# Optimization experiments

Measured on AMD Instinct MI355X. Metric: run time of the kernel, lower is better.

Reference implementation:

```python
import jax, jax.numpy as jnp
import numpy as np

N_NODES, N_EDGES, N_GRAPHS = 100000, 400000, 4096
F_NODE, F_EDGE, G = 78, 11, 256
NUM_LAYERS, NUM_TIMESTEPS = 3, 2
L = NUM_LAYERS - 1  # number of GNNLayers after GetContext


def _lrelu(x):
    return jax.nn.leaky_relu(x, 0.01)


def _seg_softmax(logits, seg, n):
    # softmax of logits grouped by segment id (edge_softmax over dst / softmax_nodes over graph)
    m = jax.ops.segment_max(logits, seg, num_segments=n)
    e = jnp.exp(logits - m[seg])
    s = jax.ops.segment_sum(e, seg, num_segments=n)
    return e / s[seg]


def _gru(x, h, Wih, Whh, bih, bhh):
    gi = x @ Wih.T + bih
    gh = h @ Whh.T + bhh
    ir, iz, inn = jnp.split(gi, 3, axis=-1)
    hr, hz, hn = jnp.split(gh, 3, axis=-1)
    r = jax.nn.sigmoid(ir + hr)
    z = jax.nn.sigmoid(iz + hz)
    nn_ = jnp.tanh(inn + r * hn)
    return (1.0 - z) * nn_ + z * h


def _forward(node_feats, edge_feats, W_pn, b_pn, W_pe1, b_pe1, W_pe2, b_pe2, W_et, b_et,
             gru0_Wih, gru0_Whh, gru0_bih, gru0_bhh,
             gnn_W_pe, gnn_b_pe, gnn_W_pn, gnn_b_pn, gnn_Wih, gnn_Whh, gnn_bih, gnn_bhh,
             ro_W_cl, ro_b_cl, ro_W_pn, ro_b_pn, ro_Wih, ro_Whh, ro_bih, ro_bhh,
             ln_gamma, ln_beta, src, dst, node_graph):
    N, B = node_feats.shape[0], N_GRAPHS
    # ---- GetContext ----
    hv_new = _lrelu(node_feats @ W_pn.T + b_pn)                                  # [N,G]
    he1 = _lrelu(jnp.concatenate([node_feats[src], edge_feats], -1) @ W_pe1.T + b_pe1)  # [E,G]
    logits = _lrelu(jnp.concatenate([hv_new[dst], he1], -1) @ W_pe2.T + b_pe2)   # [E,1]
    a = _seg_softmax(logits, dst, N)
    c = jax.ops.segment_sum(a * (he1 @ W_et.T + b_et), dst, num_segments=N)      # [N,G]
    h = jax.nn.relu(_gru(jax.nn.elu(c), hv_new, gru0_Wih, gru0_Whh, gru0_bih, gru0_bhh))
    # ---- GNNLayers (AttentiveGRU2) ----
    for l in range(L):
        lg = _lrelu(jnp.concatenate([h[dst], h[src]], -1) @ gnn_W_pe[l].T + gnn_b_pe[l])  # [E,1]
        a = _seg_softmax(lg, dst, N)
        hv = h @ gnn_W_pn[l].T + gnn_b_pn[l]
        c = jax.ops.segment_sum(a * hv[src], dst, num_segments=N)
        h = jax.nn.relu(_gru(jax.nn.elu(c), h, gnn_Wih[l], gnn_Whh[l], gnn_bih[l], gnn_bhh[l]))
    # ---- AttentiveFPReadout ----
    g_feats = jax.ops.segment_sum(h, node_graph, num_segments=B)                 # [B,G]
    for t in range(NUM_TIMESTEPS):
        z = _lrelu(jnp.concatenate([jax.nn.relu(g_feats)[node_graph], h], -1) @ ro_W_cl[t].T + ro_b_cl[t])  # [N,1]
        a = _seg_softmax(z, node_graph, B)
        hv = h @ ro_W_pn[t].T + ro_b_pn[t]
        gr = jax.ops.segment_sum(a * hv, node_graph, num_segments=B)
        g_feats = jax.nn.relu(_gru(jax.nn.elu(gr), g_feats, ro_Wih[t], ro_Whh[t], ro_bih[t], ro_bhh[t]))
    # ---- LayerNorm (dropout is identity at inference) ----
    mu = jnp.mean(g_feats, -1, keepdims=True)
    var = jnp.mean((g_feats - mu) ** 2, -1, keepdims=True)
    return (g_feats - mu) / jnp.sqrt(var + 1e-5) * ln_gamma + ln_beta


def setup_inputs() -> dict:
    key = jax.random.key(0)
    ks = iter(jax.random.split(key, 64))

    def nrm(shape, scale=1.0):
        return jax.random.normal(next(ks), shape, dtype=jnp.float32) * scale

    def lin(out_d, in_d):
        return nrm((out_d, in_d), 1.0 / np.sqrt(in_d))

    d = {}
    d['node_feats'] = nrm((N_NODES, F_NODE))
    d['edge_feats'] = nrm((N_EDGES, F_EDGE))
    d['src'] = jax.random.randint(next(ks), (N_EDGES,), 0, N_NODES)
    d['dst'] = jax.random.randint(next(ks), (N_EDGES,), 0, N_NODES)
    d['node_graph'] = jnp.sort(jax.random.randint(next(ks), (N_NODES,), 0, N_GRAPHS))
    # GetContext params
    d['W_pn'] = lin(G, F_NODE); d['b_pn'] = jnp.zeros((G,), jnp.float32)
    d['W_pe1'] = lin(G, F_NODE + F_EDGE); d['b_pe1'] = jnp.zeros((G,), jnp.float32)
    d['W_pe2'] = lin(1, 2 * G); d['b_pe2'] = jnp.zeros((1,), jnp.float32)
    d['W_et'] = lin(G, G); d['b_et'] = jnp.zeros((G,), jnp.float32)
    d['gru0_Wih'] = lin(3 * G, G); d['gru0_Whh'] = lin(3 * G, G)
    d['gru0_bih'] = jnp.zeros((3 * G,), jnp.float32); d['gru0_bhh'] = jnp.zeros((3 * G,), jnp.float32)
    # stacked GNNLayer params
    s2g = 1.0 / np.sqrt(2 * G); sg = 1.0 / np.sqrt(G)
    d['gnn_W_pe'] = nrm((L, 1, 2 * G), s2g); d['gnn_b_pe'] = jnp.zeros((L, 1), jnp.float32)
    d['gnn_W_pn'] = nrm((L, G, G), sg); d['gnn_b_pn'] = jnp.zeros((L, G), jnp.float32)
    d['gnn_Wih'] = nrm((L, 3 * G, G), sg); d['gnn_Whh'] = nrm((L, 3 * G, G), sg)
    d['gnn_bih'] = jnp.zeros((L, 3 * G), jnp.float32); d['gnn_bhh'] = jnp.zeros((L, 3 * G), jnp.float32)
    # stacked readout (GlobalPool) params
    T = NUM_TIMESTEPS
    d['ro_W_cl'] = nrm((T, 1, 2 * G), s2g); d['ro_b_cl'] = jnp.zeros((T, 1), jnp.float32)
    d['ro_W_pn'] = nrm((T, G, G), sg); d['ro_b_pn'] = jnp.zeros((T, G), jnp.float32)
    d['ro_Wih'] = nrm((T, 3 * G, G), sg); d['ro_Whh'] = nrm((T, 3 * G, G), sg)
    d['ro_bih'] = jnp.zeros((T, 3 * G), jnp.float32); d['ro_bhh'] = jnp.zeros((T, 3 * G), jnp.float32)
    d['ln_gamma'] = jnp.ones((G,), jnp.float32); d['ln_beta'] = jnp.zeros((G,), jnp.float32)
    return d


def reference(node_feats, edge_feats, src, dst, node_graph, W_pn, b_pn, W_pe1, b_pe1, W_pe2, b_pe2,
              W_et, b_et, gru0_Wih, gru0_Whh, gru0_bih, gru0_bhh,
              gnn_W_pe, gnn_b_pe, gnn_W_pn, gnn_b_pn, gnn_Wih, gnn_Whh, gnn_bih, gnn_bhh,
              ro_W_cl, ro_b_cl, ro_W_pn, ro_b_pn, ro_Wih, ro_Whh, ro_bih, ro_bhh, ln_gamma, ln_beta):
    return _forward(node_feats, edge_feats, W_pn, b_pn, W_pe1, b_pe1, W_pe2, b_pe2, W_et, b_et,
                    gru0_Wih, gru0_Whh, gru0_bih, gru0_bhh,
                    gnn_W_pe, gnn_b_pe, gnn_W_pn, gnn_b_pn, gnn_Wih, gnn_Whh, gnn_bih, gnn_bhh,
                    ro_W_cl, ro_b_cl, ro_W_pn, ro_b_pn, ro_Wih, ro_Whh, ro_bih, ro_bhh,
                    ln_gamma, ln_beta, src, dst, node_graph)
```

## Files before the change

### kernel.cpp

```cpp
#include <hip/hip_runtime.h>

#define NN 100000
#define NE 400000
#define NB 4096
#define FN 78
#define FE 11
#define GD 256
#define NL 2
#define NT 2

typedef unsigned short u16;
typedef __attribute__((ext_vector_type(8))) short bf16x8;
typedef __attribute__((ext_vector_type(4))) float f32x4;

__device__ __forceinline__ float lrelu_(float x){ return x > 0.f ? x : 0.01f*x; }
__device__ __forceinline__ float elu_(float x){ return x > 0.f ? x : expf(x) - 1.f; }
__device__ __forceinline__ float sigm_(float x){ return 1.f/(1.f + expf(-x)); }

__device__ __forceinline__ float bf2f(u16 u){ return __uint_as_float(((unsigned)u) << 16); }
__device__ __forceinline__ u16 f2bf(float f){
  unsigned u = __float_as_uint(f);
  unsigned r = (u + 0x7fffu + ((u >> 16) & 1u)) >> 16;
  return (u16)r;
}

__global__ void k_zero(float* p, size_t n){
  size_t i = (size_t)blockIdx.x*blockDim.x + threadIdx.x;
  size_t st = (size_t)gridDim.x*blockDim.x;
  for (; i < n; i += st) p[i] = 0.f;
}

__global__ void k_count(const int* __restrict__ dst, int* __restrict__ cnt, int E){
  int e = blockIdx.x*256 + threadIdx.x;
  if (e < E) atomicAdd(&cnt[dst[e]], 1);
}
__global__ void k_scan1(const int* __restrict__ cnt, int* __restrict__ part,
                        int* __restrict__ btot, int n){
  __shared__ int sd[256];
  int i = blockIdx.x*256 + threadIdx.x;
  int v = (i < n) ? cnt[i] : 0;
  sd[threadIdx.x] = v; __syncthreads();
  for (int d=1; d<256; d<<=1){
    int t = (threadIdx.x >= d) ? sd[threadIdx.x-d] : 0;
    __syncthreads();
    sd[threadIdx.x] += t;
    __syncthreads();
  }
  if (i < n) part[i] = sd[threadIdx.x];
  if (threadIdx.x == 255) btot[blockIdx.x] = sd[255];
}
__global__ void k_scan2(const int* __restrict__ btot, int* __restrict__ boff, int nb){
  __shared__ int sd[512];
  int tid = threadIdx.x;
  int v = (tid < nb) ? btot[tid] : 0;
  sd[tid] = v; __syncthreads();
  for (int d=1; d<512; d<<=1){
    int t = (tid >= d) ? sd[tid-d] : 0;
    __syncthreads();
    sd[tid] += t;
    __syncthreads();
  }
  if (tid < nb) boff[tid] = sd[tid] - v;
}
__global__ void k_scan3(const int* __restrict__ part, const int* __restrict__ boff,
                        int* __restrict__ rowptr, int n){
  int i = blockIdx.x*256 + threadIdx.x;
  if (i < n) rowptr[i+1] = part[i] + boff[blockIdx.x];
  if (i == 0) rowptr[0] = 0;
}
__global__ void k_cursor(const int* __restrict__ rowptr, int* __restrict__ cursor, int n){
  int i = blockIdx.x*256 + threadIdx.x;
  if (i < n) cursor[i] = rowptr[i];
}
__global__ void k_fill(const int* __restrict__ dst, int* __restrict__ cursor,
                       int* __restrict__ order, int E){
  int e = blockIdx.x*256 + threadIdx.x;
  if (e < E){
    int pos = atomicAdd(&cursor[dst[e]], 1);
    order[pos] = e;
  }
}
__global__ void k_gpb(const int* __restrict__ ng, int* __restrict__ gpb, int N, int B){
  int b = blockIdx.x*256 + threadIdx.x;
  if (b > B) return;
  int lo = 0, hi = N;
  while (lo < hi){ int mid = (lo+hi)>>1; if (ng[mid] < b) lo = mid+1; else hi = mid; }
  gpb[b] = lo;
}

__global__ void k_pack_b(const float* __restrict__ W, u16* __restrict__ Bp, int OUT, int K){
  int t = blockIdx.x*256 + threadIdx.x;
  if (t >= OUT*K) return;
  int j = t & 7;
  int l = (t >> 3) & 63;
  int rest = t >> 9;
  int nks = K >> 5;
  int ks = rest % nks, c = rest / nks;
  int col = c*16 + (l & 15);
  int k = ks*32 + (l >> 4)*8 + j;
  Bp[t] = f2bf(W[(size_t)col*K + k]);
}

__global__ void k_pack_b96(const float* __restrict__ W, int ldw, u16* __restrict__ Bp){
  int t = blockIdx.x*256 + threadIdx.x;
  if (t >= 256*96) return;
  int j = t & 7;
  int l = (t >> 3) & 63;
  int rest = t >> 9;
  int ks = rest % 3, c = rest / 3;
  int col = c*16 + (l & 15);
  int k = ks*32 + (l >> 4)*8 + j;
  Bp[t] = (k < FN) ? f2bf(W[(size_t)col*ldw + k]) : (u16)0;
}

__global__ void k_pack_rz(const float* __restrict__ Wih, const float* __restrict__ Whh,
                          u16* __restrict__ Bp){
  int t = blockIdx.x*256 + threadIdx.x;
  int j = t & 7;
  int l = (t >> 3) & 63;
  int rest = t >> 9;
  int ks = rest & 15, c = rest >> 4;
  int srcrow = (c & 1)*256 + (c >> 1)*16 + (l & 15);
  int k = ks*32 + (l >> 4)*8 + j;
  float v = (k < 256) ? Wih[(size_t)srcrow*GD + k] : Whh[(size_t)srcrow*GD + (k - 256)];
  Bp[t] = f2bf(v);
}

__global__ void __launch_bounds__(512)
k_np2_mfma(const float* __restrict__ nf,
           const u16* __restrict__ BpA, const float* __restrict__ bA,
           const u16* __restrict__ BpB, const float* __restrict__ bB,
           u16* __restrict__ hv, u16* __restrict__ Pb, int N){
  int tid = threadIdx.x;
  int wv = __builtin_amdgcn_readfirstlane(tid >> 6);
  int lane = tid & 63;
  int m = lane & 15, kg = lane >> 4;
  int r0 = blockIdx.x*64;
  f32x4 accA[2][4], accB[2][4];
  #pragma unroll
  for (int t=0;t<2;t++)
    #pragma unroll
    for (int rt=0;rt<4;rt++){ accA[t][rt] = (f32x4)(0.f); accB[t][rt] = (f32x4)(0.f); }
  #pragma unroll
  for (int ks=0; ks<3; ks++){
    int koff = ks*32 + kg*8;
    bf16x8 a[4];
    #pragma unroll
    for (int rt=0; rt<4; rt++){
      int row = r0 + rt*16 + m;
      if (row > N-1) row = N-1;
      const float* base = nf + (size_t)row*FN;
      #pragma unroll
      for (int q=0;q<8;q++){
        int k = koff + q;
        a[rt][q] = (short)((k < FN) ? f2bf(base[k]) : (u16)0);
      }
    }
    #pragma unroll
    for (int t=0;t<2;t++){
      int c = wv*2 + t;
      bf16x8 bva = *(const bf16x8*)&BpA[(size_t)((c*3 + ks)*64 + lane)*8];
      bf16x8 bvb = *(const bf16x8*)&BpB[(size_t)((c*3 + ks)*64 + lane)*8];
      #pragma unroll
      for (int rt=0; rt<4; rt++){
        accA[t][rt] = __builtin_amdgcn_mfma_f32_16x16x32_bf16(a[rt], bva, accA[t][rt], 0, 0, 0);
        accB[t][rt] = __builtin_amdgcn_mfma_f32_16x16x32_bf16(a[rt], bvb, accB[t][rt], 0, 0, 0);
      }
    }
  }
  #pragma unroll
  for (int t=0;t<2;t++){
    int col = wv*32 + t*16 + m;
    float ba = bA[col], bb = bB[col];
    #pragma unroll
    for (int rt=0; rt<4; rt++){
      #pragma unroll
      for (int i=0;i<4;i++){
        int row = r0 + rt*16 + kg*4 + i;
        if (row < N){
          hv[(size_t)row*GD + col] = f2bf(lrelu_(accA[t][rt][i] + ba));
          Pb[(size_t)row*GD + col] = f2bf(accB[t][rt][i] + bb);
        }
      }
    }
  }
}

__global__ void k_dot2_bf16(const u16* __restrict__ rows, const float* __restrict__ wv,
                            float* __restrict__ za, float* __restrict__ zb, int N){
  int wav = threadIdx.x >> 6, lane = threadIdx.x & 63;
  int i = blockIdx.x*4 + wav;
  if (i >= N) return;
  int c0 = lane*4;
  ushort4 r4 = *(const ushort4*)&rows[(size_t)i*GD + c0];
  float4 wa = *(const float4*)&wv[c0];
  float4 wb = *(const float4*)&wv[GD + c0];
  float v0 = bf2f(r4.x), v1 = bf2f(r4.y), v2 = bf2f(r4.z), v3 = bf2f(r4.w);
  float va = v0*wa.x + v1*wa.y + v2*wa.z + v3*wa.w;
  float vb = v0*wb.x + v1*wb.y + v2*wb.z + v3*wb.w;
  #pragma unroll
  for (int off=32; off; off>>=1){ va += __shfl_down(va, off); vb += __shfl_down(vb, off); }
  if (lane == 0){ za[i] = va; zb[i] = vb; }
}

__global__ void k_dot1_bf16(const u16* __restrict__ rows, const float* __restrict__ wv,
                            float* __restrict__ z, int N){
  int wav = threadIdx.x >> 6, lane = threadIdx.x & 63;
  int i = blockIdx.x*4 + wav;
  if (i >= N) return;
  int c0 = lane*4;
  ushort4 r4 = *(const ushort4*)&rows[(size_t)i*GD + c0];
  float4 wa = *(const float4*)&wv[c0];
  float va = bf2f(r4.x)*wa.x + bf2f(r4.y)*wa.y + bf2f(r4.z)*wa.z + bf2f(r4.w)*wa.w;
  #pragma unroll
  for (int off=32; off; off>>=1) va += __shfl_down(va, off);
  if (lane == 0) z[i] = va;
}

__global__ void k_dotg_relu(const float* __restrict__ g, const float* __restrict__ wv,
                            float* __restrict__ zg, int B){
  int wav = threadIdx.x >> 6, lane = threadIdx.x & 63;
  int i = blockIdx.x*4 + wav;
  if (i >= B) return;
  int c0 = lane*4;
  float4 gv = *(const float4*)&g[(size_t)i*GD + c0];
  float4 wa = *(const float4*)&wv[c0];
  float va = fmaxf(gv.x,0.f)*wa.x + fmaxf(gv.y,0.f)*wa.y + fmaxf(gv.z,0.f)*wa.z + fmaxf(gv.w,0.f)*wa.w;
  #pragma unroll
  for (int off=32; off; off>>=1) va += __shfl_down(va, off);
  if (lane == 0) zg[i] = va;
}

__global__ void __launch_bounds__(256)
k_ctx_fused(const u16* __restrict__ P, const float* __restrict__ za,
            const int* __restrict__ order, const int* __restrict__ rowptr,
            const int* __restrict__ src, const float* __restrict__ ef,
            const float* __restrict__ Wpe1, const float* __restrict__ bpe1,
            const float* __restrict__ Wpe2, const float* __restrict__ bpe2,
            u16* __restrict__ wc, float* __restrict__ sdeg, int N){
  int wv = threadIdx.x >> 6, lane = threadIdx.x & 63;
  int d = blockIdx.x*4 + wv;
  if (d >= N) return;
  int j0 = rowptr[d], j1 = rowptr[d+1];
  int c0 = lane*4;
  float wb0 = Wpe2[GD+c0], wb1 = Wpe2[GD+c0+1], wb2 = Wpe2[GD+c0+2], wb3 = Wpe2[GD+c0+3];
  float bp0 = bpe1[c0], bp1 = bpe1[c0+1], bp2 = bpe1[c0+2], bp3 = bpe1[c0+3];
  float wk0[FE], wk1[FE], wk2[FE], wk3[FE];
  #pragma unroll
  for (int k=0;k<FE;k++){
    wk0[k] = Wpe1[(size_t)(c0+0)*(FN+FE) + FN + k];
    wk1[k] = Wpe1[(size_t)(c0+1)*(FN+FE) + FN + k];
    wk2[k] = Wpe1[(size_t)(c0+2)*(FN+FE) + FN + k];
    wk3[k] = Wpe1[(size_t)(c0+3)*(FN+FE) + FN + k];
  }
  float zad = za[d] + bpe2[0];
  float m = -1e30f, s = 0.f;
  float a0=0.f, a1=0.f, a2=0.f, a3=0.f;
  for (int j=j0; j<j1; j++){
    int e = order[j];
    int sn = src[e];
    ushort4 p4 = *(const ushort4*)&P[(size_t)sn*GD + c0];
    const float* efp = &ef[(size_t)e*FE];
    float efv[FE];
    #pragma unroll
    for (int k=0;k<FE;k++) efv[k] = efp[k];
    float h0 = bf2f(p4.x)+bp0, h1 = bf2f(p4.y)+bp1, h2 = bf2f(p4.z)+bp2, h3 = bf2f(p4.w)+bp3;
    #pragma unroll
    for (int k=0;k<FE;k++){
      h0 += wk0[k]*efv[k]; h1 += wk1[k]*efv[k]; h2 += wk2[k]*efv[k]; h3 += wk3[k]*efv[k];
    }
    h0 = lrelu_(h0); h1 = lrelu_(h1); h2 = lrelu_(h2); h3 = lrelu_(h3);
    float part = h0*wb0 + h1*wb1 + h2*wb2 + h3*wb3;
    #pragma unroll
    for (int off=32; off; off>>=1) part += __shfl_down(part, off);
    float l = lrelu_(part + zad);
    l = __shfl(l, 0);
    float mn = fmaxf(m, l);
    float sc = __expf(m - mn);
    float p  = __expf(l - mn);
    s = s*sc + p;
    a0 = a0*sc + p*h0; a1 = a1*sc + p*h1; a2 = a2*sc + p*h2; a3 = a3*sc + p*h3;
    m = mn;
  }
  float inv = (j1 > j0) ? 1.f/s : 0.f;
  ushort4 o;
  o.x = f2bf(a0*inv); o.y = f2bf(a1*inv); o.z = f2bf(a2*inv); o.w = f2bf(a3*inv);
  *(ushort4*)&wc[(size_t)d*GD + c0] = o;
  if (lane == 0) sdeg[d] = (j1 > j0) ? 1.f : 0.f;
}

__global__ void __launch_bounds__(256)
k_gnn_fused(const u16* __restrict__ hv, const float* __restrict__ za, const float* __restrict__ zb,
            const int* __restrict__ order, const int* __restrict__ rowptr,
            const int* __restrict__ src, const float* __restrict__ bias,
            u16* __restrict__ cw, int N){
  int wv = threadIdx.x >> 6, lane = threadIdx.x & 63;
  int d = blockIdx.x*4 + wv;
  if (d >= N) return;
  int j0 = rowptr[d], j1 = rowptr[d+1];
  int c0 = lane*4;
  float zad = za[d] + bias[0];
  float M = -1e30f;
  for (int j=j0; j<j1; j++){
    int sn = src[order[j]];
    M = fmaxf(M, lrelu_(zad + zb[sn]));
  }
  float s = 0.f;
  float a0=0.f, a1=0.f, a2=0.f, a3=0.f;
  for (int j=j0; j<j1; j++){
    int e = order[j];
    int sn = src[e];
    float p = __expf(lrelu_(zad + zb[sn]) - M);
    ushort4 r4 = *(const ushort4*)&hv[(size_t)sn*GD + c0];
    s += p;
    a0 += p*bf2f(r4.x);
    a1 += p*bf2f(r4.y);
    a2 += p*bf2f(r4.z);
    a3 += p*bf2f(r4.w);
  }
  float inv = (j1 > j0) ? 1.f/s : 0.f;
  ushort4 o;
  o.x = f2bf(elu_(a0*inv)); o.y = f2bf(elu_(a1*inv));
  o.z = f2bf(elu_(a2*inv)); o.w = f2bf(elu_(a3*inv));
  *(ushort4*)&cw[(size_t)d*GD + c0] = o;
}

__global__ void __launch_bounds__(256)
k_ro_fused(const u16* __restrict__ hv, const float* __restrict__ zg, const float* __restrict__ zh,
           const int* __restrict__ gpb, const float* __restrict__ bias,
           float* __restrict__ gr, int B){
  int b = blockIdx.x, tid = threadIdx.x;
  int i0 = gpb[b], i1 = gpb[b+1];
  float zgb = zg[b] + bias[0];
  __shared__ float red[256];
  float lm = -1e30f;
  for (int i = i0 + tid; i < i1; i += 256) lm = fmaxf(lm, lrelu_(zgb + zh[i]));
  red[tid] = lm; __syncthreads();
  for (int d2=128; d2; d2>>=1){ if (tid < d2) red[tid] = fmaxf(red[tid], red[tid+d2]); __syncthreads(); }
  float M = red[0]; __syncthreads();
  float ls = 0.f;
  for (int i = i0 + tid; i < i1; i += 256) ls += __expf(lrelu_(zgb + zh[i]) - M);
  red[tid] = ls; __syncthreads();
  for (int d2=128; d2; d2>>=1){ if (tid < d2) red[tid] += red[tid+d2]; __syncthreads(); }
  float S = red[0];
  float acc = 0.f;
  for (int i = i0; i < i1; i++){
    float p = __expf(lrelu_(zgb + zh[i]) - M);
    acc += p * bf2f(hv[(size_t)i*GD + tid]);
  }
  gr[(size_t)b*GD + tid] = (i1 > i0) ? acc/S : 0.f;
}

__global__ void k_segsum_sorted(const u16* __restrict__ h, const int* __restrict__ gpb,
                                float* __restrict__ g, int B){
  int b = blockIdx.x, tid = threadIdx.x;
  int i0 = gpb[b], i1 = gpb[b+1];
  float acc = 0.f;
  for (int i = i0; i < i1; i++) acc += bf2f(h[(size_t)i*GD + tid]);
  g[(size_t)b*GD + tid] = acc;
}

__global__ void __launch_bounds__(512)
k_gru_mfma32(const u16* __restrict__ x, const u16* __restrict__ hprev,
             const u16* __restrict__ rzp, const u16* __restrict__ nip, const u16* __restrict__ nhp,
             const float* __restrict__ bih, const float* __restrict__ bhh,
             u16* __restrict__ hout, int R){
  int tid = threadIdx.x;
  int wv = __builtin_amdgcn_readfirstlane(tid >> 6);
  int lane = tid & 63;
  int m = lane & 15, kg = lane >> 4;
  int r0 = blockIdx.x*32;

  f32x4 arz[2][4], ani[2][2], anh[2][2];
  #pragma unroll
  for (int rt=0;rt<2;rt++){
    #pragma unroll
    for (int t=0;t<4;t++) arz[rt][t] = (f32x4)(0.f);
    #pragma unroll
    for (int t=0;t<2;t++){ ani[rt][t] = (f32x4)(0.f); anh[rt][t] = (f32x4)(0.f); }
  }

  #pragma unroll
  for (int ks=0; ks<8; ks++){
    int koff = ks*32 + kg*8;
    bf16x8 ax[2], ah[2];
    #pragma unroll
    for (int rt=0; rt<2; rt++){
      int row = r0 + rt*16 + m;
      ax[rt] = *(const bf16x8*)&x[(size_t)row*GD + koff];
      ah[rt] = *(const bf16x8*)&hprev[(size_t)row*GD + koff];
    }
    #pragma unroll
    for (int t=0;t<4;t++){
      int c = wv*4 + t;
      bf16x8 bx = *(const bf16x8*)&rzp[(size_t)((c*16 + ks    )*64 + lane)*8];
      bf16x8 bh = *(const bf16x8*)&rzp[(size_t)((c*16 + ks + 8)*64 + lane)*8];
      #pragma unroll
      for (int rt=0; rt<2; rt++){
        arz[rt][t] = __builtin_amdgcn_mfma_f32_16x16x32_bf16(ax[rt], bx, arz[rt][t], 0, 0, 0);
        arz[rt][t] = __builtin_amdgcn_mfma_f32_16x16x32_bf16(ah[rt], bh, arz[rt][t], 0, 0, 0);
      }
    }
    #pragma unroll
    for (int t=0;t<2;t++){
      int c = wv*2 + t;
      bf16x8 bi = *(const bf16x8*)&nip[(size_t)((c*8 + ks)*64 + lane)*8];
      bf16x8 bh = *(const bf16x8*)&nhp[(size_t)((c*8 + ks)*64 + lane)*8];
      #pragma unroll
      for (int rt=0; rt<2; rt++){
        ani[rt][t] = __builtin_amdgcn_mfma_f32_16x16x32_bf16(ax[rt], bi, ani[rt][t], 0, 0, 0);
        anh[rt][t] = __builtin_amdgcn_mfma_f32_16x16x32_bf16(ah[rt], bh, anh[rt][t], 0, 0, 0);
      }
    }
  }

  #pragma unroll
  for (int g=0; g<2; g++){
    int ch = (wv*2 + g)*16 + m;
    float brz_r = bih[ch] + bhh[ch];
    float brz_z = bih[ch+GD] + bhh[ch+GD];
    float bin   = bih[ch+2*GD];
    float bhn   = bhh[ch+2*GD];
    #pragma unroll
    for (int rt=0; rt<2; rt++){
      #pragma unroll
      for (int i=0;i<4;i++){
        int row = r0 + rt*16 + kg*4 + i;
        float rr = sigm_(arz[rt][2*g  ][i] + brz_r);
        float zz = sigm_(arz[rt][2*g+1][i] + brz_z);
        float nn = tanhf(ani[rt][g][i] + bin + rr*(anh[rt][g][i] + bhn));
        float hp = bf2f(hprev[(size_t)row*GD + ch]);
        float o = (1.f - zz)*nn + zz*hp;
        hout[(size_t)row*GD + ch] = f2bf(fmaxf(o, 0.f));
      }
    }
  }
}

template<int DO_ELU>
__global__ void __launch_bounds__(512)
k_proj_mfma64(const u16* __restrict__ X, const u16* __restrict__ Wp,
              const float* __restrict__ b, u16* __restrict__ Y, int R,
              const float* __restrict__ mask){
  int tid = threadIdx.x;
  int wv = __builtin_amdgcn_readfirstlane(tid >> 6);
  int lane = tid & 63;
  int m = lane & 15, kg = lane >> 4;
  int r0 = blockIdx.x*64;
  f32x4 acc[2][4];
  #pragma unroll
  for (int t=0;t<2;t++)
    #pragma unroll
    for (int rt=0;rt<4;rt++) acc[t][rt] = (f32x4)(0.f);
  #pragma unroll
  for (int ks=0; ks<8; ks++){
    int koff = ks*32 + kg*8;
    bf16x8 a[4];
    #pragma unroll
    for (int rt=0; rt<4; rt++){
      int row = r0 + rt*16 + m;
      if (row > R-1) row = R-1;
      a[rt] = *(const bf16x8*)&X[(size_t)row*GD + koff];
    }
    #pragma unroll
    for (int t=0;t<2;t++){
      int c = wv*2 + t;
      bf16x8 bv = *(const bf16x8*)&Wp[(size_t)((c*8 + ks)*64 + lane)*8];
      #pragma unroll
      for (int rt=0; rt<4; rt++)
        acc[t][rt] = __builtin_amdgcn_mfma_f32_16x16x32_bf16(a[rt], bv, acc[t][rt], 0, 0, 0);
    }
  }
  #pragma unroll
  for (int t=0;t<2;t++){
    int col = wv*32 + t*16 + m;
    float bb = b[col];
    #pragma unroll
    for (int rt=0; rt<4; rt++){
      #pragma unroll
      for (int i=0;i<4;i++){
        int row = r0 + rt*16 + kg*4 + i;
        if (row < R){
          float v = acc[t][rt][i] + bb;
          if (DO_ELU){
            float mk = (mask[row] > 0.f) ? 1.f : 0.f;
            v = elu_(v*mk);
          }
          Y[(size_t)row*GD + col] = f2bf(v);
        }
      }
    }
  }
}

__global__ void __launch_bounds__(256)
k_gru_mfma_f32(const float* __restrict__ x, const float* __restrict__ hprev,
               const u16* __restrict__ Wihp, const u16* __restrict__ Whhp,
               const float* __restrict__ bih, const float* __restrict__ bhh,
               float* __restrict__ hout, int R){
  int tid = threadIdx.x;
  int wave = __builtin_amdgcn_readfirstlane(tid >> 6);
  int lane = tid & 63;
  int m = lane & 15, kg = lane >> 4;
  int r0 = blockIdx.x*16;

  f32x4 agi[3][4], agh[3][4];
  #pragma unroll
  for (int g=0;g<3;g++)
    #pragma unroll
    for (int t=0;t<4;t++){ agi[g][t] = (f32x4)(0.f); agh[g][t] = (f32x4)(0.f); }

  #pragma unroll
  for (int ks=0; ks<8; ks++){
    int koff = ks*32 + kg*8;
    const float* xp = x + (size_t)(r0 + m)*GD + koff;
    float4 x0 = *(const float4*)xp;
    float4 x1 = *(const float4*)(xp+4);
    bf16x8 ax;
    ax[0]=(short)f2bf(elu_(x0.x)); ax[1]=(short)f2bf(elu_(x0.y));
    ax[2]=(short)f2bf(elu_(x0.z)); ax[3]=(short)f2bf(elu_(x0.w));
    ax[4]=(short)f2bf(elu_(x1.x)); ax[5]=(short)f2bf(elu_(x1.y));
    ax[6]=(short)f2bf(elu_(x1.z)); ax[7]=(short)f2bf(elu_(x1.w));
    const float* hr = hprev + (size_t)(r0 + m)*GD + koff;
    float4 h0 = *(const float4*)hr;
    float4 h1 = *(const float4*)(hr+4);
    bf16x8 ah;
    ah[0]=(short)f2bf(h0.x); ah[1]=(short)f2bf(h0.y); ah[2]=(short)f2bf(h0.z); ah[3]=(short)f2bf(h0.w);
    ah[4]=(short)f2bf(h1.x); ah[5]=(short)f2bf(h1.y); ah[6]=(short)f2bf(h1.z); ah[7]=(short)f2bf(h1.w);
    #pragma unroll
    for (int g=0;g<3;g++){
      #pragma unroll
      for (int t=0;t<4;t++){
        int c = g*16 + wave*4 + t;
        bf16x8 bi = *(const bf16x8*)&Wihp[(size_t)((c*8 + ks)*64 + lane)*8];
        bf16x8 bh = *(const bf16x8*)&Whhp[(size_t)((c*8 + ks)*64 + lane)*8];
        agi[g][t] = __builtin_amdgcn_mfma_f32_16x16x32_bf16(ax, bi, agi[g][t], 0, 0, 0);
        agh[g][t] = __builtin_amdgcn_mfma_f32_16x16x32_bf16(ah, bh, agh[g][t], 0, 0, 0);
      }
    }
  }
  #pragma unroll
  for (int t=0;t<4;t++){
    int col = wave*64 + t*16 + m;
    float bir = bih[col],      bhr = bhh[col];
    float biz = bih[col+GD],   bhz = bhh[col+GD];
    float bin = bih[col+2*GD], bhn = bhh[col+2*GD];
    #pragma unroll
    for (int i=0;i<4;i++){
      int row = r0 + kg*4 + i;
      float rr = sigm_(agi[0][t][i] + bir + agh[0][t][i] + bhr);
      float zz = sigm_(agi[1][t][i] + biz + agh[1][t][i] + bhz);
      float nn = tanhf(agi[2][t][i] + bin + rr*(agh[2][t][i] + bhn));
      float hp = hprev[(size_t)row*GD + col];
      float o = (1.f - zz)*nn + zz*hp;
      hout[(size_t)row*GD + col] = fmaxf(o, 0.f);
    }
  }
}

__global__ void k_layernorm(const float* __restrict__ gb, const float* __restrict__ gamma,
                            const float* __restrict__ beta, float* __restrict__ outb){
  int r = blockIdx.x, j = threadIdx.x;
  float v = gb[(size_t)r*GD + j];
  float s1 = v, s2 = v*v;
  #pragma unroll
  for (int off=32; off; off>>=1){ s1 += __shfl_down(s1, off); s2 += __shfl_down(s2, off); }
  __shared__ float r1[4], r2[4];
  int wv = j >> 6, lane = j & 63;
  if (lane == 0){ r1[wv] = s1; r2[wv] = s2; }
  __syncthreads();
  float S1 = r1[0]+r1[1]+r1[2]+r1[3];
  float S2 = r2[0]+r2[1]+r2[2]+r2[3];
  float mu = S1/(float)GD;
  float var = fmaxf(S2/(float)GD - mu*mu, 0.f);
  outb[(size_t)r*GD + j] = (v - mu)/sqrtf(var + 1e-5f)*gamma[j] + beta[j];
}

extern "C" void kernel_launch(void* const* d_in, const int* in_sizes, int n_in,
                              void* d_out, int out_size, void* d_ws, size_t ws_size,
                              hipStream_t stream){
  const float* node_feats = (const float*)d_in[0];
  const float* edge_feats = (const float*)d_in[1];
  const int*   src        = (const int*)d_in[2];
  const int*   dst        = (const int*)d_in[3];
  const int*   node_graph = (const int*)d_in[4];
  const float* W_pn   = (const float*)d_in[5];
  const float* b_pn   = (const float*)d_in[6];
  const float* W_pe1  = (const float*)d_in[7];
  const float* b_pe1  = (const float*)d_in[8];
  const float* W_pe2  = (const float*)d_in[9];
  const float* b_pe2  = (const float*)d_in[10];
  const float* W_et   = (const float*)d_in[11];
  const float* b_et   = (const float*)d_in[12];
  const float* g0_Wih = (const float*)d_in[13];
  const float* g0_Whh = (const float*)d_in[14];
  const float* g0_bih = (const float*)d_in[15];
  const float* g0_bhh = (const float*)d_in[16];
  const float* gnn_W_pe = (const float*)d_in[17];
  const float* gnn_b_pe = (const float*)d_in[18];
  const float* gnn_W_pn = (const float*)d_in[19];
  const float* gnn_b_pn = (const float*)d_in[20];
  const float* gnn_Wih  = (const float*)d_in[21];
  const float* gnn_Whh  = (const float*)d_in[22];
  const float* gnn_bih  = (const float*)d_in[23];
  const float* gnn_bhh  = (const float*)d_in[24];
  const float* ro_W_cl = (const float*)d_in[25];
  const float* ro_b_cl = (const float*)d_in[26];
  const float* ro_W_pn = (const float*)d_in[27];
  const float* ro_b_pn = (const float*)d_in[28];
  const float* ro_Wih  = (const float*)d_in[29];
  const float* ro_Whh  = (const float*)d_in[30];
  const float* ro_bih  = (const float*)d_in[31];
  const float* ro_bhh  = (const float*)d_in[32];
  const float* ln_gamma = (const float*)d_in[33];
  const float* ln_beta  = (const float*)d_in[34];
  float* outp = (float*)d_out;

  const int NBLK = (NN + 255)/256;

  char* w = (char*)d_ws;
  size_t need = 0;
  float* gbuf  = (float*)(w + need); need += (size_t)NB*GD*4;
  float* grbuf = (float*)(w + need); need += (size_t)NB*GD*4;
  float* za    = (float*)(w + need); need += (size_t)NN*4;
  float* zb    = (float*)(w + need); need += (size_t)NN*4;
  float* zg    = (float*)(w + need); need += (size_t)NB*4;
  float* sdeg  = (float*)(w + need); need += (size_t)NN*4;
  int*   cnt    = (int*)(w + need); need += (size_t)NN*4;
  int*   rowptr = (int*)(w + need); need += (size_t)(NN+1)*4;
  int*   cursor = (int*)(w + need); need += (size_t)NN*4;
  int*   order  = (int*)(w + need); need += (size_t)NE*4;
  int*   gpb    = (int*)(w + need); need += (size_t)(NB+1)*4;
  int*   btot   = (int*)(w + need); need += (size_t)512*4;
  int*   boff   = (int*)(w + need); need += (size_t)512*4;
  u16*   hbuf = (u16*)(w + need); need += (size_t)NN*GD*2;
  u16*   htmp = (u16*)(w + need); need += (size_t)NN*GD*2;
  u16*   cwb  = (u16*)(w + need); need += (size_t)NN*GD*2;
  u16*   dbuf = (u16*)(w + need); need += (size_t)NN*GD*2;
  u16* pGruN = (u16*)(w + need); need += (size_t)3*393216*2;
  u16* pGruR = (u16*)(w + need); need += (size_t)4*196608*2;
  u16* pPn  = (u16*)(w + need); need += (size_t)4*GD*GD*2;
  u16* pEt  = (u16*)(w + need); need += (size_t)GD*GD*2;
  u16* pNp  = (u16*)(w + need); need += (size_t)2*256*96*2;
  if (ws_size < need) return;
  u16* Pbuf   = hbuf;
  u16* hv_new = htmp;

  const size_t LW = 393216;
  const size_t OW = 196608;
  const size_t PW = (size_t)GD*GD;
  const size_t NPW = (size_t)256*96;
  const int G64 = (NN + 63)/64;
  const int G32 = NN/32;

  k_zero<<<64, 256, 0, stream>>>((float*)cnt, (size_t)NN);
  k_count<<<(NE+255)/256, 256, 0, stream>>>(dst, cnt, NE);
  k_scan1<<<NBLK, 256, 0, stream>>>(cnt, cnt, btot, NN);
  k_scan2<<<1, 512, 0, stream>>>(btot, boff, NBLK);
  k_scan3<<<NBLK, 256, 0, stream>>>(cnt, boff, rowptr, NN);
  k_cursor<<<NBLK, 256, 0, stream>>>(rowptr, cursor, NN);
  k_fill<<<(NE+255)/256, 256, 0, stream>>>(dst, cursor, order, NE);
  k_gpb<<<(NB+256)/256, 256, 0, stream>>>(node_graph, gpb, NN, NB);

  const float* wihs[3] = { g0_Wih, gnn_Wih, gnn_Wih + (size_t)3*GD*GD };
  const float* whhs[3] = { g0_Whh, gnn_Whh, gnn_Whh + (size_t)3*GD*GD };
  for (int l=0;l<3;l++){
    k_pack_rz<<<1024, 256, 0, stream>>>(wihs[l], whhs[l], pGruN + l*LW);
    k_pack_b<<<256, 256, 0, stream>>>(wihs[l] + (size_t)512*GD, pGruN + l*LW + 262144, 256, GD);
    k_pack_b<<<256, 256, 0, stream>>>(whhs[l] + (size_t)512*GD, pGruN + l*LW + 327680, 256, GD);
  }
  for (int t=0;t<NT;t++){
    k_pack_b<<<768, 256, 0, stream>>>(ro_Wih + (size_t)t*3*GD*GD, pGruR + (2*t)*OW, 768, GD);
    k_pack_b<<<768, 256, 0, stream>>>(ro_Whh + (size_t)t*3*GD*GD, pGruR + (2*t+1)*OW, 768, GD);
  }
  for (int l=0;l<NL;l++)
    k_pack_b<<<256, 256, 0, stream>>>(gnn_W_pn + (size_t)l*GD*GD, pPn + l*PW, GD, GD);
  for (int t=0;t<NT;t++)
    k_pack_b<<<256, 256, 0, stream>>>(ro_W_pn + (size_t)t*GD*GD, pPn + (2+t)*PW, GD, GD);
  k_pack_b<<<256, 256, 0, stream>>>(W_et, pEt, GD, GD);
  k_pack_b96<<<96, 256, 0, stream>>>(W_pn, FN, pNp);
  k_pack_b96<<<96, 256, 0, stream>>>(W_pe1, FN+FE, pNp + NPW);

  k_np2_mfma<<<G64, 512, 0, stream>>>(node_feats, pNp, b_pn, pNp + NPW, b_pe1,
                                      hv_new, Pbuf, NN);
  k_dot1_bf16<<<(NN+3)/4, 256, 0, stream>>>(hv_new, W_pe2, za, NN);
  k_ctx_fused<<<(NN+3)/4, 256, 0, stream>>>(Pbuf, za, order, rowptr, src, edge_feats,
                                            W_pe1, b_pe1, W_pe2, b_pe2, cwb, sdeg, NN);
  k_proj_mfma64<1><<<G64, 512, 0, stream>>>(cwb, pEt, b_et, dbuf, NN, sdeg);
  k_gru_mfma32<<<G32, 512, 0, stream>>>(dbuf, hv_new, pGruN + 0*LW, pGruN + 0*LW + 262144,
                                        pGruN + 0*LW + 327680, g0_bih, g0_bhh, hbuf, NN);

  for (int l=0; l<NL; l++){
    k_dot2_bf16<<<(NN+3)/4, 256, 0, stream>>>(hbuf, gnn_W_pe + (size_t)l*2*GD, za, zb, NN);
    k_proj_mfma64<0><<<G64, 512, 0, stream>>>(hbuf, pPn + l*PW, gnn_b_pn + (size_t)l*GD,
                                              htmp, NN, nullptr);
    k_gnn_fused<<<(NN+3)/4, 256, 0, stream>>>(htmp, za, zb, order, rowptr, src,
                                              gnn_b_pe + l, cwb, NN);
    k_gru_mfma32<<<G32, 512, 0, stream>>>(cwb, hbuf,
                                pGruN + (1+l)*LW, pGruN + (1+l)*LW + 262144, pGruN + (1+l)*LW + 327680,
                                gnn_bih + (size_t)l*3*GD, gnn_bhh + (size_t)l*3*GD, hbuf, NN);
  }

  k_segsum_sorted<<<NB, 256, 0, stream>>>(hbuf, gpb, gbuf, NB);
  for (int t=0; t<NT; t++){
    k_dotg_relu<<<(NB+3)/4, 256, 0, stream>>>(gbuf, ro_W_cl + (size_t)t*2*GD, zg, NB);
    k_dot1_bf16<<<(NN+3)/4, 256, 0, stream>>>(hbuf, ro_W_cl + (size_t)t*2*GD + GD, za, NN);
    k_proj_mfma64<0><<<G64, 512, 0, stream>>>(hbuf, pPn + (2+t)*PW, ro_b_pn + (size_t)t*GD,
                                              htmp, NN, nullptr);
    k_ro_fused<<<NB, 256, 0, stream>>>(htmp, zg, za, gpb, ro_b_cl + t, grbuf, NB);
    k_gru_mfma_f32<<<NB/16, 256, 0, stream>>>(grbuf, gbuf,
                                pGruR + (2*t)*OW, pGruR + (2*t+1)*OW,
                                ro_bih + (size_t)t*3*GD, ro_bhh + (size_t)t*3*GD, gbuf, NB);
  }
  k_layernorm<<<NB, 256, 0, stream>>>(gbuf, ln_gamma, ln_beta, outp);
}
```

Measured before the change: 1.969 ms.

## Split context attention into edge-parallel he1 kernel and per-node aggregation

Replaces the fused per-destination context kernel with two kernels. The first computes he1 and the attention logit per edge in dst-sorted order, writing he1 to a bf16 buffer. The second does a per-node softmax and weighted aggregation over contiguous rows. This is meant to fix load imbalance and poor parallelism in the fused per-node loop, at the cost of writing and re-reading a 400k x 256 bf16 intermediate (~200MB of traffic). The new path runs only when the workspace is large enough; otherwise the old fused kernel is used.

```diff
diff --git a/kernel.cpp b/kernel.cpp
--- a/kernel.cpp
+++ b/kernel.cpp
@@ -229,6 +229,81 @@
   #pragma unroll
   for (int off=32; off; off>>=1) va += __shfl_down(va, off);
   if (lane == 0) zg[i] = va;
+}
+
+__global__ void __launch_bounds__(256)
+k_he1s(const u16* __restrict__ P, const float* __restrict__ za,
+       const int* __restrict__ order, const int* __restrict__ src, const int* __restrict__ dst,
+       const float* __restrict__ ef, const float* __restrict__ Wpe1,
+       const float* __restrict__ bpe1, const float* __restrict__ Wpe2,
+       const float* __restrict__ bpe2, u16* __restrict__ he1s, float* __restrict__ lg, int E){
+  int wv = threadIdx.x >> 6, lane = threadIdx.x & 63;
+  int jbase = (blockIdx.x*4 + wv)*8;
+  if (jbase >= E) return;
+  int c0 = lane*4;
+  float wb0 = Wpe2[GD+c0], wb1 = Wpe2[GD+c0+1], wb2 = Wpe2[GD+c0+2], wb3 = Wpe2[GD+c0+3];
+  float bp0 = bpe1[c0], bp1 = bpe1[c0+1], bp2 = bpe1[c0+2], bp3 = bpe1[c0+3];
+  float wk0[FE], wk1[FE], wk2[FE], wk3[FE];
+  #pragma unroll
+  for (int k=0;k<FE;k++){
+    wk0[k] = Wpe1[(size_t)(c0+0)*(FN+FE) + FN + k];
+    wk1[k] = Wpe1[(size_t)(c0+1)*(FN+FE) + FN + k];
+    wk2[k] = Wpe1[(size_t)(c0+2)*(FN+FE) + FN + k];
+    wk3[k] = Wpe1[(size_t)(c0+3)*(FN+FE) + FN + k];
+  }
+  float b2 = bpe2[0];
+  for (int jj=0; jj<8; jj++){
+    int j = jbase + jj; if (j >= E) break;
+    int e = order[j];
+    int sn = src[e], d = dst[e];
+    ushort4 p4 = *(const ushort4*)&P[(size_t)sn*GD + c0];
+    const float* efp = &ef[(size_t)e*FE];
+    float efv[FE];
+    #pragma unroll
+    for (int k=0;k<FE;k++) efv[k] = efp[k];
+    float h0 = bf2f(p4.x)+bp0, h1 = bf2f(p4.y)+bp1, h2 = bf2f(p4.z)+bp2, h3 = bf2f(p4.w)+bp3;
+    #pragma unroll
+    for (int k=0;k<FE;k++){
+      h0 += wk0[k]*efv[k]; h1 += wk1[k]*efv[k]; h2 += wk2[k]*efv[k]; h3 += wk3[k]*efv[k];
+    }
+    h0 = lrelu_(h0); h1 = lrelu_(h1); h2 = lrelu_(h2); h3 = lrelu_(h3);
+    ushort4 o;
+    o.x = f2bf(h0); o.y = f2bf(h1); o.z = f2bf(h2); o.w = f2bf(h3);
+    *(ushort4*)&he1s[(size_t)j*GD + c0] = o;
+    float part = h0*wb0 + h1*wb1 + h2*wb2 + h3*wb3;
+    #pragma unroll
+    for (int off=32; off; off>>=1) part += __shfl_down(part, off);
+    if (lane == 0) lg[j] = lrelu_(part + za[d] + b2);
+  }
+}
+
+__global__ void __launch_bounds__(256)
+k_ctx_agg(const u16* __restrict__ he1s, const float* __restrict__ lg,
+          const int* __restrict__ rowptr, u16* __restrict__ wc,
+          float* __restrict__ sdeg, int N){
+  int wv = threadIdx.x >> 6, lane = threadIdx.x & 63;
+  int d = blockIdx.x*4 + wv;
+  if (d >= N) return;
+  int j0 = rowptr[d], j1 = rowptr[d+1];
+  int c0 = lane*4;
+  float M = -1e30f;
+  for (int j=j0; j<j1; j++) M = fmaxf(M, lg[j]);
+  float s = 0.f;
+  float a0=0.f, a1=0.f, a2=0.f, a3=0.f;
+  for (int j=j0; j<j1; j++){
+    float p = __expf(lg[j] - M);
+    ushort4 h4 = *(const ushort4*)&he1s[(size_t)j*GD + c0];
+    s += p;
+    a0 += p*bf2f(h4.x);
+    a1 += p*bf2f(h4.y);
+    a2 += p*bf2f(h4.z);
+    a3 += p*bf2f(h4.w);
+  }
+  float inv = (j1 > j0) ? 1.f/s : 0.f;
+  ushort4 o;
+  o.x = f2bf(a0*inv); o.y = f2bf(a1*inv); o.z = f2bf(a2*inv); o.w = f2bf(a3*inv);
+  *(ushort4*)&wc[(size_t)d*GD + c0] = o;
+  if (lane == 0) sdeg[d] = (j1 > j0) ? 1.f : 0.f;
 }
 
 __global__ void __launch_bounds__(256)
@@ -626,6 +701,7 @@
   float* zb    = (float*)(w + need); need += (size_t)NN*4;
   float* zg    = (float*)(w + need); need += (size_t)NB*4;
   float* sdeg  = (float*)(w + need); need += (size_t)NN*4;
+  float* lg    = (float*)(w + need); need += (size_t)NE*4;
   int*   cnt    = (int*)(w + need); need += (size_t)NN*4;
   int*   rowptr = (int*)(w + need); need += (size_t)(NN+1)*4;
   int*   cursor = (int*)(w + need); need += (size_t)NN*4;
@@ -643,6 +719,8 @@
   u16* pEt  = (u16*)(w + need); need += (size_t)GD*GD*2;
   u16* pNp  = (u16*)(w + need); need += (size_t)2*256*96*2;
   if (ws_size < need) return;
+  u16* he1s = (u16*)(w + need);
+  bool use_sorted = (ws_size >= need + (size_t)NE*GD*2);
   u16* Pbuf   = hbuf;
   u16* hv_new = htmp;
 
@@ -684,8 +762,14 @@
   k_np2_mfma<<<G64, 512, 0, stream>>>(node_feats, pNp, b_pn, pNp + NPW, b_pe1,
                                       hv_new, Pbuf, NN);
   k_dot1_bf16<<<(NN+3)/4, 256, 0, stream>>>(hv_new, W_pe2, za, NN);
-  k_ctx_fused<<<(NN+3)/4, 256, 0, stream>>>(Pbuf, za, order, rowptr, src, edge_feats,
-                                            W_pe1, b_pe1, W_pe2, b_pe2, cwb, sdeg, NN);
+  if (use_sorted){
+    k_he1s<<<NE/32, 256, 0, stream>>>(Pbuf, za, order, src, dst, edge_feats,
+                                      W_pe1, b_pe1, W_pe2, b_pe2, he1s, lg, NE);
+    k_ctx_agg<<<(NN+3)/4, 256, 0, stream>>>(he1s, lg, rowptr, cwb, sdeg, NN);
+  } else {
+    k_ctx_fused<<<(NN+3)/4, 256, 0, stream>>>(Pbuf, za, order, rowptr, src, edge_feats,
+                                              W_pe1, b_pe1, W_pe2, b_pe2, cwb, sdeg, NN);
+  }
   k_proj_mfma64<1><<<G64, 512, 0, stream>>>(cwb, pEt, b_et, dbuf, NN, sdeg);
   k_gru_mfma32<<<G32, 512, 0, stream>>>(dbuf, hv_new, pGruN + 0*LW, pGruN + 0*LW + 262144,
                                         pGruN + 0*LW + 327680, g0_bih, g0_bhh, hbuf, NN);
```

Measured after the change: 1.966 ms. About the same (-0.1%).
